# Kernel optimization log

Hardware: AMD Instinct MI355X
Metric: run time of the kernel (lower is better)

Reference implementation:

```python
import jax, jax.numpy as jnp
import numpy as np

N_NODES = 25000
N_HEDGES = 12500
NNZ = 400000
C_IN = 128
HID = 256
HEADS = 4
DH = HID // HEADS  # 64
NQ = 1             # number_queries
LN_EPS = 1e-5


def _layer_norm(x, g, b):
    m = jnp.mean(x, axis=-1, keepdims=True)
    v = jnp.mean((x - m) ** 2, axis=-1, keepdims=True)
    return (x - m) * jax.lax.rsqrt(v + LN_EPS) * g + b


def _block(x_src, src, tgt, n_tgt, K, Qw, V, ln0_g, ln0_b, ln1_g, ln1_b, W1, W2):
    """AllSetTransformerBlock: segment-softmax multi-head attention + LN/MLP.

    x_src: [N_src, C]; K,V: [H, C, DH]; Qw: [H, NQ, DH]; src,tgt: [E] int.
    torch.sparse.softmax over dim=1 == softmax over each target's incident
    sources (unspecified entries are -inf), so a segment softmax is exact.
    """
    xK = jnp.einsum('nc,hcd->hnd', x_src, K)        # [H, N, DH]
    alpha = jnp.einsum('hqd,hnd->nhq', Qw, xK)      # [N, H, NQ]
    a = alpha[src]                                   # [E, H, NQ] gather per incidence
    m = jax.ops.segment_max(a, tgt, num_segments=n_tgt)
    e = jnp.exp(a - m[tgt])
    den = jax.ops.segment_sum(e, tgt, num_segments=n_tgt)
    attn = e / den[tgt]                              # [E, H, NQ]
    v = jnp.einsum('nc,hcd->nhd', x_src, V)[src]     # [E, H, DH]
    w = attn[:, :, :, None] * v[:, :, None, :]       # [E, H, NQ, DH]
    out = jax.ops.segment_sum(w, tgt, num_segments=n_tgt)  # [T, H, NQ, DH]
    out = out + Qw[None]                             # residual with queries
    out = out.transpose(0, 2, 1, 3).reshape(n_tgt, NQ, HID)
    x = _layer_norm(out, ln0_g, ln0_b)
    h = jnp.maximum(x @ W1, 0.0) @ W2                # MLP: Linear-ReLU-Linear, no bias
    x = _layer_norm(x + jnp.maximum(h, 0.0), ln1_g, ln1_b)
    return x.sum(axis=1)                             # [T, HID]


def setup_inputs() -> dict:
    key = jax.random.key(0)
    ks = jax.random.split(key, 12)
    # injective linear-congruential index generation -> unique (node, hedge) pairs,
    # matching a coalesced sparse incidence matrix
    P = 15485863
    lin = (np.arange(NNZ, dtype=np.int64) * P) % (N_NODES * N_HEDGES)
    node_idx = jnp.asarray(lin // N_HEDGES, dtype=jnp.int64)
    hedge_idx = jnp.asarray(lin % N_HEDGES, dtype=jnp.int64)
    s = 0.05
    w = lambda k, shape: jax.random.normal(k, shape, jnp.float32) * s
    d = {
        'x0': jax.random.normal(ks[0], (N_NODES, C_IN), jnp.float32),
        'node_idx': node_idx,
        'hedge_idx': hedge_idx,
        'n_hedges': N_HEDGES,
        'v2e_K': w(ks[1], (HEADS, C_IN, DH)),
        'v2e_Q': w(ks[2], (HEADS, NQ, DH)),
        'v2e_V': w(ks[3], (HEADS, C_IN, DH)),
        'v2e_W1': w(ks[4], (HID, HID)),
        'v2e_W2': w(ks[5], (HID, HID)),
        'v2e_ln0_g': jnp.ones(HID, jnp.float32), 'v2e_ln0_b': jnp.zeros(HID, jnp.float32),
        'v2e_ln1_g': jnp.ones(HID, jnp.float32), 'v2e_ln1_b': jnp.zeros(HID, jnp.float32),
        'e2v_K': w(ks[6], (HEADS, HID, DH)),
        'e2v_Q': w(ks[7], (HEADS, NQ, DH)),
        'e2v_V': w(ks[8], (HEADS, HID, DH)),
        'e2v_W1': w(ks[9], (HID, HID)),
        'e2v_W2': w(ks[10], (HID, HID)),
        'e2v_ln0_g': jnp.ones(HID, jnp.float32), 'e2v_ln0_b': jnp.zeros(HID, jnp.float32),
        'e2v_ln1_g': jnp.ones(HID, jnp.float32), 'e2v_ln1_b': jnp.zeros(HID, jnp.float32),
    }
    return d


def reference(x0, node_idx, hedge_idx, n_hedges,
              v2e_K, v2e_Q, v2e_V, v2e_W1, v2e_W2,
              v2e_ln0_g, v2e_ln0_b, v2e_ln1_g, v2e_ln1_b,
              e2v_K, e2v_Q, e2v_V, e2v_W1, e2v_W2,
              e2v_ln0_g, e2v_ln0_b, e2v_ln1_g, e2v_ln1_b):
    n_nodes = x0.shape[0]
    # vertex -> hyperedge (neighborhood = B^T: targets are hyperedges)
    x1 = jax.nn.relu(_block(x0, node_idx, hedge_idx, n_hedges,
                            v2e_K, v2e_Q, v2e_V,
                            v2e_ln0_g, v2e_ln0_b, v2e_ln1_g, v2e_ln1_b,
                            v2e_W1, v2e_W2))
    # hyperedge -> vertex (neighborhood = B: targets are nodes)
    x0_out = jax.nn.relu(_block(x1, hedge_idx, node_idx, n_nodes,
                                e2v_K, e2v_Q, e2v_V,
                                e2v_ln0_g, e2v_ln0_b, e2v_ln1_g, e2v_ln1_b,
                                e2v_W1, e2v_W2))
    return x0_out, x1
```

## Files before the change

### kernel.cpp

```cpp
#include <hip/hip_runtime.h>
#include <hip/hip_bf16.h>

#define N_NODES_C 25000
#define N_HEDGES_C 12500
#define NNZ_C 400000
#define C_IN_C 128
#define HID_C 256
#define LN_EPS_C 1e-5f
#define CSR_STRIDE 64

typedef unsigned short ushort_t;
typedef __attribute__((ext_vector_type(8))) short short8;
typedef __attribute__((ext_vector_type(4))) float f32x4;

union U4S8 { uint4 u; short8 s; };

__device__ __forceinline__ float ldsel(const void* p, size_t i, bool f32) {
    return f32 ? ((const float*)p)[i] : __bfloat162float(((const __hip_bfloat16*)p)[i]);
}
__device__ __forceinline__ int ldidx(const void* p, size_t i, bool i64) {
    return i64 ? (int)((const long long*)p)[i] : ((const int*)p)[i];
}
__device__ __forceinline__ ushort_t bfbits(float f) {
    union { float f; unsigned u; } v; v.f = f;
    unsigned r = v.u + 0x7FFF + ((v.u >> 16) & 1);
    return (ushort_t)(r >> 16);
}
__device__ __forceinline__ float blo(unsigned u) {
    union { unsigned u; float f; } v; v.u = u << 16; return v.f;
}
__device__ __forceinline__ float bhi(unsigned u) {
    union { unsigned u; float f; } v; v.u = u & 0xFFFF0000u; return v.f;
}

#define INIT_GRID 3273
__global__ void __launch_bounds__(256)
init_kernel(const unsigned* __restrict__ x0w, const unsigned* __restrict__ idxw,
            int* __restrict__ flags, unsigned* __restrict__ cnts,
            unsigned* __restrict__ scsrh32, unsigned* __restrict__ scsrn32,
            unsigned* __restrict__ vb32, unsigned* __restrict__ ea32) {
    int bid = blockIdx.x;
    if (bid == 0) {
        __shared__ int cnt[2];
        int t = threadIdx.x;
        if (t < 2) cnt[t] = 0;
        __syncthreads();
        int c0 = 0, c1 = 0;
        for (int k = 0; k < 4; k++) {
            unsigned w = x0w[t * 4 + k];
            unsigned elo = (w >> 7) & 0xFF;
            if (elo >= 100 && elo <= 134) c0++;
            if (idxw[2 * (t * 4 + k) + 1] == 0) c1++;
        }
        atomicAdd(&cnt[0], c0);
        atomicAdd(&cnt[1], c1);
        __syncthreads();
        if (t == 0) {
            flags[0] = (cnt[0] < 512) ? 1 : 0;
            flags[1] = (cnt[1] >= 512) ? 1 : 0;
        }
        return;
    }
    int i = (bid - 1) * 256 + threadIdx.x;
    if (i < 37500) { cnts[i] = 0u; return; }
    i -= 37500;
    if (i < 400000) { scsrh32[i] = 0x61A861A8u; return; }
    i -= 400000;
    if (i < 400000) { scsrn32[i] = 0x30D430D4u; return; }
    i -= 400000;
    if (i < 128) { vb32[25000 * 128 + i] = 0u; return; }
    i -= 128;
    if (i < 4) ea32[100000 + i] = 0u;
}

#define PREP_TOTAL 364544
__global__ void prep_kernel(const void* __restrict__ K1, const void* __restrict__ Q1,
                            const void* __restrict__ V1,
                            const void* __restrict__ K2, const void* __restrict__ Q2,
                            const void* __restrict__ V2,
                            const void* __restrict__ W1a, const void* __restrict__ W2a,
                            const void* __restrict__ W1b, const void* __restrict__ W2b,
                            const void* __restrict__ G0a, const void* __restrict__ B0a,
                            const void* __restrict__ G1a, const void* __restrict__ B1a,
                            const void* __restrict__ G0b, const void* __restrict__ B0b,
                            const void* __restrict__ G1b, const void* __restrict__ B1b,
                            const int* __restrict__ flags,
                            float* __restrict__ kq1, float* __restrict__ kq2,
                            ushort_t* __restrict__ Vt1b, ushort_t* __restrict__ Vt2b,
                            ushort_t* __restrict__ W1tA, ushort_t* __restrict__ W2tA,
                            ushort_t* __restrict__ W1tB, ushort_t* __restrict__ W2tB,
                            float* __restrict__ qgb1, float* __restrict__ ep1,
                            float* __restrict__ qgb2, float* __restrict__ ep2) {
    bool f32 = flags[0] != 0;
    size_t i = (size_t)blockIdx.x * 256 + threadIdx.x;
    if (i >= PREP_TOTAL) return;
    if (i < 512) {
        int h = (int)(i >> 7), c = (int)(i & 127);
        float s = 0.f;
        for (int d = 0; d < 64; d++)
            s += ldsel(K1, (size_t)(h * 128 + c) * 64 + d, f32) * ldsel(Q1, h * 64 + d, f32);
        kq1[h * 128 + c] = s;
        return;
    }
    i -= 512;
    if (i < 1024) {
        int h = (int)(i >> 8), c = (int)(i & 255);
        float s = 0.f;
        for (int d = 0; d < 64; d++)
            s += ldsel(K2, (size_t)(h * 256 + c) * 64 + d, f32) * ldsel(Q2, h * 64 + d, f32);
        kq2[h * 256 + c] = s;
        return;
    }
    i -= 1024;
    if (i < 32768) {
        int j = (int)(i >> 7), c = (int)(i & 127);
        int h = j >> 6, d = j & 63;
        Vt1b[i] = bfbits(ldsel(V1, (size_t)(h * 128 + c) * 64 + d, f32));
        return;
    }
    i -= 32768;
    if (i < 65536) {
        int j = (int)(i >> 8), c = (int)(i & 255);
        int h = j >> 6, d = j & 63;
        Vt2b[i] = bfbits(ldsel(V2, (size_t)(h * 256 + c) * 64 + d, f32));
        return;
    }
    i -= 65536;
    if (i < 65536) { int n = (int)(i >> 8), k = (int)(i & 255);
        W1tA[i] = bfbits(ldsel(W1a, (size_t)k * 256 + n, f32)); return; }
    i -= 65536;
    if (i < 65536) { int n = (int)(i >> 8), k = (int)(i & 255);
        W2tA[i] = bfbits(ldsel(W2a, (size_t)k * 256 + n, f32)); return; }
    i -= 65536;
    if (i < 65536) { int n = (int)(i >> 8), k = (int)(i & 255);
        W1tB[i] = bfbits(ldsel(W1b, (size_t)k * 256 + n, f32)); return; }
    i -= 65536;
    if (i < 65536) { int n = (int)(i >> 8), k = (int)(i & 255);
        W2tB[i] = bfbits(ldsel(W2b, (size_t)k * 256 + n, f32)); return; }
    i -= 65536;
    {
        int which = (int)(i >> 8);
        int j = (int)(i & 255);
        const void* src; float* dst;
        switch (which) {
            case 0: src = Q1;  dst = qgb1;       break;
            case 1: src = G0a; dst = qgb1 + 256; break;
            case 2: src = B0a; dst = qgb1 + 512; break;
            case 3: src = G1a; dst = ep1;        break;
            case 4: src = B1a; dst = ep1 + 256;  break;
            case 5: src = Q2;  dst = qgb2;       break;
            case 6: src = G0b; dst = qgb2 + 256; break;
            case 7: src = B0b; dst = qgb2 + 512; break;
            case 8: src = G1b; dst = ep2;        break;
            default: src = B1b; dst = ep2 + 256;  break;
        }
        dst[j] = ldsel(src, j, f32);
    }
}

#define FILL_CHUNK 1024
#define FILL_NCHUNK ((NNZ_C + FILL_CHUNK - 1) / FILL_CHUNK)
#define HSLICE_SZ 1563
#define NSLICE_SZ 3125
__global__ void __launch_bounds__(256)
fill_kernel(const void* __restrict__ node_idx, const void* __restrict__ hedge_idx,
            const int* __restrict__ flags,
            int* __restrict__ fill_h, int* __restrict__ fill_n,
            ushort_t* __restrict__ scsr_h, ushort_t* __restrict__ scsr_n) {
    bool i64 = flags[1] != 0;
    int s = blockIdx.x & 7;
    int chunk = blockIdx.x >> 3;
    int e0 = chunk * FILL_CHUNK;
    int e1 = e0 + FILL_CHUNK; if (e1 > NNZ_C) e1 = NNZ_C;
    int hlo = s * HSLICE_SZ, hhi = hlo + HSLICE_SZ;
    int nlo = s * NSLICE_SZ, nhi = nlo + NSLICE_SZ;
    for (int e = e0 + threadIdx.x; e < e1; e += 256) {
        int nd = ldidx(node_idx, e, i64);
        int he = ldidx(hedge_idx, e, i64);
        if (he >= hlo && he < hhi) {
            int p = atomicAdd(&fill_h[he], 1);
            if (p < CSR_STRIDE) scsr_h[(he << 6) + p] = (ushort_t)nd;
        }
        if (nd >= nlo && nd < nhi) {
            int p = atomicAdd(&fill_n[nd], 1);
            if (p < CSR_STRIDE) scsr_n[(nd << 6) + p] = (ushort_t)he;
        }
    }
}

__device__ __forceinline__ void gemm_mfma_body(
    const ushort_t* __restrict__ Abf, const float* __restrict__ Af32,
    const ushort_t* __restrict__ Bt, ushort_t* __restrict__ Cout,
    int M, int K, int row0, int col0, int relu, ushort_t* As, ushort_t* Bs) {
    int tid = threadIdx.x;
    int w = tid >> 6, lane = tid & 63;
    int l15 = lane & 15, kg = lane >> 4;
    int wr = w >> 1, wc = w & 1;
    f32x4 acc[2][4] = {{{0.f,0.f,0.f,0.f},{0.f,0.f,0.f,0.f},{0.f,0.f,0.f,0.f},{0.f,0.f,0.f,0.f}},
                       {{0.f,0.f,0.f,0.f},{0.f,0.f,0.f,0.f},{0.f,0.f,0.f,0.f},{0.f,0.f,0.f,0.f}}};
    for (int k0 = 0; k0 < K; k0 += 64) {
#pragma unroll
        for (int p = 0; p < 2; p++) {
            int i = p * 256 + tid;
            int r = i >> 3, ch = i & 7;
            uint4 av = {0u,0u,0u,0u};
            int gr = row0 + r;
            if (gr < M) {
                if (Abf) {
                    av = *(const uint4*)(Abf + (size_t)gr * K + k0 + ch * 8);
                } else {
                    const float* ap = Af32 + (size_t)gr * K + k0 + ch * 8;
                    float4 f0 = *(const float4*)ap;
                    float4 f1 = *(const float4*)(ap + 4);
                    av.x = (unsigned)bfbits(f0.x) | ((unsigned)bfbits(f0.y) << 16);
                    av.y = (unsigned)bfbits(f0.z) | ((unsigned)bfbits(f0.w) << 16);
                    av.z = (unsigned)bfbits(f1.x) | ((unsigned)bfbits(f1.y) << 16);
                    av.w = (unsigned)bfbits(f1.z) | ((unsigned)bfbits(f1.w) << 16);
                }
            }
            *(uint4*)&As[r * 72 + ch * 8] = av;
        }
#pragma unroll
        for (int p = 0; p < 4; p++) {
            int i = p * 256 + tid;
            int r2 = i >> 3, c2 = i & 7;
            uint4 bv = *(const uint4*)(Bt + (size_t)(col0 + r2) * K + k0 + c2 * 8);
            *(uint4*)&Bs[r2 * 72 + c2 * 8] = bv;
        }
        __syncthreads();
#pragma unroll
        for (int kk = 0; kk < 2; kk++) {
            U4S8 a0_, a1_;
            a0_.u = *(const uint4*)&As[(32 * wr + l15) * 72 + kk * 32 + kg * 8];
            a1_.u = *(const uint4*)&As[(32 * wr + 16 + l15) * 72 + kk * 32 + kg * 8];
#pragma unroll
            for (int n = 0; n < 4; n++) {
                U4S8 b; b.u = *(const uint4*)&Bs[(64 * wc + 16 * n + l15) * 72 + kk * 32 + kg * 8];
                acc[0][n] = __builtin_amdgcn_mfma_f32_16x16x32_bf16(a0_.s, b.s, acc[0][n], 0, 0, 0);
                acc[1][n] = __builtin_amdgcn_mfma_f32_16x16x32_bf16(a1_.s, b.s, acc[1][n], 0, 0, 0);
            }
        }
        __syncthreads();
    }
#pragma unroll
    for (int m = 0; m < 2; m++) {
#pragma unroll
        for (int n = 0; n < 4; n++) {
#pragma unroll
            for (int rr = 0; rr < 4; rr++) {
                int row = row0 + 32 * wr + 16 * m + kg * 4 + rr;
                if (row < M) {
                    float v = acc[m][n][rr];
                    if (relu) v = fmaxf(v, 0.f);
                    Cout[(size_t)row * 256 + col0 + 64 * wc + 16 * n + l15] = bfbits(v);
                }
            }
        }
    }
}

__global__ void __launch_bounds__(256)
gemm_bf16_kernel(const ushort_t* __restrict__ A, const ushort_t* __restrict__ Bt,
                 ushort_t* __restrict__ C, int M, int K, int relu) {
    __shared__ ushort_t As[64 * 72];
    __shared__ ushort_t Bs[128 * 72];
    gemm_mfma_body(A, nullptr, Bt, C, M, K, blockIdx.x * 64, blockIdx.y * 128, relu, As, Bs);
}

__global__ void __launch_bounds__(256)
gemm_x0_kernel(const void* __restrict__ x0, const int* __restrict__ flags,
               const ushort_t* __restrict__ Bt, ushort_t* __restrict__ C,
               int M, int K) {
    __shared__ ushort_t As[64 * 72];
    __shared__ ushort_t Bs[128 * 72];
    bool f32 = flags[0] != 0;
    gemm_mfma_body(f32 ? nullptr : (const ushort_t*)x0,
                   f32 ? (const float*)x0 : nullptr,
                   Bt, C, M, K, blockIdx.x * 64, blockIdx.y * 128, 0, As, Bs);
}

__global__ void __launch_bounds__(512)
fused_mlp_ln_kernel(const ushort_t* __restrict__ A, const ushort_t* __restrict__ W1t,
                    const ushort_t* __restrict__ W2t, const float* __restrict__ ep,
                    float* __restrict__ outF, ushort_t* __restrict__ xbfOut, int M) {
    __shared__ ushort_t Bs[256 * 72];
    __shared__ ushort_t hs[64 * 264];
    __shared__ float s1s[64][4];
    __shared__ float s2s[64][4];
    ushort_t* As = hs;
    int tid = threadIdx.x;
    int w = tid >> 6, lane = tid & 63;
    int l15 = lane & 15, kg = lane >> 4;
    int wr = w >> 2, wc = w & 3;
    int row0 = blockIdx.x * 64;
    f32x4 acc[2][4] = {{{0.f,0.f,0.f,0.f},{0.f,0.f,0.f,0.f},{0.f,0.f,0.f,0.f},{0.f,0.f,0.f,0.f}},
                       {{0.f,0.f,0.f,0.f},{0.f,0.f,0.f,0.f},{0.f,0.f,0.f,0.f},{0.f,0.f,0.f,0.f}}};
    int r = tid >> 3, ch = tid & 7;
    for (int k0 = 0; k0 < 256; k0 += 64) {
        uint4 av = {0u,0u,0u,0u};
        int gr = row0 + r;
        if (gr < M) av = *(const uint4*)(A + (size_t)gr * 256 + k0 + ch * 8);
        *(uint4*)&As[r * 72 + ch * 8] = av;
#pragma unroll
        for (int p = 0; p < 4; p++) {
            int i = p * 512 + tid;
            int r2 = i >> 3, c2 = i & 7;
            uint4 bv = *(const uint4*)(W1t + (size_t)r2 * 256 + k0 + c2 * 8);
            *(uint4*)&Bs[r2 * 72 + c2 * 8] = bv;
        }
        __syncthreads();
#pragma unroll
        for (int kk = 0; kk < 2; kk++) {
            U4S8 a0_, a1_;
            a0_.u = *(const uint4*)&As[(32 * wr + l15) * 72 + kk * 32 + kg * 8];
            a1_.u = *(const uint4*)&As[(32 * wr + 16 + l15) * 72 + kk * 32 + kg * 8];
#pragma unroll
            for (int n = 0; n < 4; n++) {
                U4S8 b; b.u = *(const uint4*)&Bs[(64 * wc + 16 * n + l15) * 72 + kk * 32 + kg * 8];
                acc[0][n] = __builtin_amdgcn_mfma_f32_16x16x32_bf16(a0_.s, b.s, acc[0][n], 0, 0, 0);
                acc[1][n] = __builtin_amdgcn_mfma_f32_16x16x32_bf16(a1_.s, b.s, acc[1][n], 0, 0, 0);
            }
        }
        __syncthreads();
    }
#pragma unroll
    for (int m = 0; m < 2; m++) {
#pragma unroll
        for (int n = 0; n < 4; n++) {
#pragma unroll
            for (int rr = 0; rr < 4; rr++) {
                int br = 32 * wr + 16 * m + kg * 4 + rr;
                hs[br * 264 + 64 * wc + 16 * n + l15] = bfbits(fmaxf(acc[m][n][rr], 0.f));
                acc[m][n][rr] = 0.f;
            }
        }
    }
    __syncthreads();
    for (int k0 = 0; k0 < 256; k0 += 64) {
#pragma unroll
        for (int p = 0; p < 4; p++) {
            int i = p * 512 + tid;
            int r2 = i >> 3, c2 = i & 7;
            uint4 bv = *(const uint4*)(W2t + (size_t)r2 * 256 + k0 + c2 * 8);
            *(uint4*)&Bs[r2 * 72 + c2 * 8] = bv;
        }
        __syncthreads();
#pragma unroll
        for (int kk = 0; kk < 2; kk++) {
            U4S8 a0_, a1_;
            a0_.u = *(const uint4*)&hs[(32 * wr + l15) * 264 + k0 + kk * 32 + kg * 8];
            a1_.u = *(const uint4*)&hs[(32 * wr + 16 + l15) * 264 + k0 + kk * 32 + kg * 8];
#pragma unroll
            for (int n = 0; n < 4; n++) {
                U4S8 b; b.u = *(const uint4*)&Bs[(64 * wc + 16 * n + l15) * 72 + kk * 32 + kg * 8];
                acc[0][n] = __builtin_amdgcn_mfma_f32_16x16x32_bf16(a0_.s, b.s, acc[0][n], 0, 0, 0);
                acc[1][n] = __builtin_amdgcn_mfma_f32_16x16x32_bf16(a1_.s, b.s, acc[1][n], 0, 0, 0);
            }
        }
        __syncthreads();
    }
    float ym[2][4][4];
#pragma unroll
    for (int m = 0; m < 2; m++) {
#pragma unroll
        for (int rr = 0; rr < 4; rr++) {
            int br = 32 * wr + 16 * m + kg * 4 + rr;
            int grow = row0 + br;
            float ls1 = 0.f;
#pragma unroll
            for (int n = 0; n < 4; n++) {
                int col = 64 * wc + 16 * n + l15;
                float xv = 0.f;
                if (grow < M) xv = blo((unsigned)A[(size_t)grow * 256 + col]);
                float yv = xv + fmaxf(acc[m][n][rr], 0.f);
                ym[m][n][rr] = yv;
                ls1 += yv;
            }
#pragma unroll
            for (int msk = 1; msk < 16; msk <<= 1) ls1 += __shfl_xor(ls1, msk);
            if (l15 == 0) s1s[br][wc] = ls1;
        }
    }
    __syncthreads();
    float mean_[2][4];
#pragma unroll
    for (int m = 0; m < 2; m++) {
#pragma unroll
        for (int rr = 0; rr < 4; rr++) {
            int br = 32 * wr + 16 * m + kg * 4 + rr;
            float mn = (s1s[br][0] + s1s[br][1] + s1s[br][2] + s1s[br][3]) * (1.f / 256.f);
            mean_[m][rr] = mn;
            float ls2 = 0.f;
#pragma unroll
            for (int n = 0; n < 4; n++) {
                float d = ym[m][n][rr] - mn;
                ls2 += d * d;
            }
#pragma unroll
            for (int msk = 1; msk < 16; msk <<= 1) ls2 += __shfl_xor(ls2, msk);
            if (l15 == 0) s2s[br][wc] = ls2;
        }
    }
    __syncthreads();
#pragma unroll
    for (int m = 0; m < 2; m++) {
#pragma unroll
        for (int rr = 0; rr < 4; rr++) {
            int br = 32 * wr + 16 * m + kg * 4 + rr;
            int grow = row0 + br;
            float var = (s2s[br][0] + s2s[br][1] + s2s[br][2] + s2s[br][3]) * (1.f / 256.f);
            float rs = rsqrtf(var + LN_EPS_C);
            if (grow < M) {
#pragma unroll
                for (int n = 0; n < 4; n++) {
                    int col = 64 * wc + 16 * n + l15;
                    float rv = (ym[m][n][rr] - mean_[m][rr]) * rs * ep[col] + ep[256 + col];
                    rv = fmaxf(rv, 0.f);
                    outF[(size_t)grow * 256 + col] = rv;
                    if (xbfOut) xbfOut[(size_t)grow * 256 + col] = bfbits(rv);
                }
            }
        }
    }
}

__global__ void __launch_bounds__(256)
expalpha_kernel(const void* __restrict__ x, int mode,
                const int* __restrict__ flags,
                const float* __restrict__ kq,
                float* __restrict__ ea, int M, int C,
                unsigned* __restrict__ zrow, float* __restrict__ zea) {
    __shared__ float kqs[1024];
    if (blockIdx.x == gridDim.x - 1) {
        int t = threadIdx.x;
        if (zrow) {
            if (t < 128) zrow[t] = 0u;
            else if (t < 132) zea[t - 128] = 0.f;
        }
        return;
    }
    bool xf32 = mode ? false : (flags[0] != 0);
    for (int i = threadIdx.x; i < 4 * C; i += 256) kqs[i] = kq[i];
    __syncthreads();
    int lane = threadIdx.x & 63;
    int n = blockIdx.x * 4 + (threadIdx.x >> 6);
    if (n >= M) return;
    float s0, s1, s2, s3;
    if (xf32) {
        float2 v = *(const float2*)((const float*)x + (size_t)n * C + lane * 2);
        int c = lane * 2;
        s0 = v.x * kqs[c]         + v.y * kqs[c + 1];
        s1 = v.x * kqs[C + c]     + v.y * kqs[C + c + 1];
        s2 = v.x * kqs[2 * C + c] + v.y * kqs[2 * C + c + 1];
        s3 = v.x * kqs[3 * C + c] + v.y * kqs[3 * C + c + 1];
    } else if (C == 128) {
        unsigned u = *((const unsigned*)x + (size_t)n * 64 + lane);
        float xl = blo(u), xh = bhi(u);
        int c = lane * 2;
        s0 = xl * kqs[c]         + xh * kqs[c + 1];
        s1 = xl * kqs[C + c]     + xh * kqs[C + c + 1];
        s2 = xl * kqs[2 * C + c] + xh * kqs[2 * C + c + 1];
        s3 = xl * kqs[3 * C + c] + xh * kqs[3 * C + c + 1];
    } else {
        uint2 u = *((const uint2*)x + (size_t)n * 64 + lane);
        float x0v = blo(u.x), x1v = bhi(u.x), x2v = blo(u.y), x3v = bhi(u.y);
        int c = lane * 4;
        s0 = x0v * kqs[c]         + x1v * kqs[c + 1]         + x2v * kqs[c + 2]         + x3v * kqs[c + 3];
        s1 = x0v * kqs[C + c]     + x1v * kqs[C + c + 1]     + x2v * kqs[C + c + 2]     + x3v * kqs[C + c + 3];
        s2 = x0v * kqs[2 * C + c] + x1v * kqs[2 * C + c + 1] + x2v * kqs[2 * C + c + 2] + x3v * kqs[2 * C + c + 3];
        s3 = x0v * kqs[3 * C + c] + x1v * kqs[3 * C + c + 1] + x2v * kqs[3 * C + c + 2] + x3v * kqs[3 * C + c + 3];
    }
#pragma unroll
    for (int m = 32; m; m >>= 1) {
        s0 += __shfl_xor(s0, m);
        s1 += __shfl_xor(s1, m);
        s2 += __shfl_xor(s2, m);
        s3 += __shfl_xor(s3, m);
    }
    if (lane == 0) {
        float4 o;
        o.x = __expf(s0); o.y = __expf(s1); o.z = __expf(s2); o.w = __expf(s3);
        *(float4*)(ea + (size_t)n * 4) = o;
    }
}

#define DECL_BANKD(B) float e##B##0, e##B##1, e##B##2, e##B##3; \
                      uint2 u##B##0, u##B##1, u##B##2, u##B##3;
#define ISSUED1(B, n, sl) { int _o = __shfl(myidx, (sl)) << 9; \
    u##B##n = *(const uint2*)(vbL + _o); \
    e##B##n = *(const float*)(eaL + (_o >> 5)); }
#define ISSUED4(B, base) ISSUED1(B,0,(base)) ISSUED1(B,1,(base)+1) ISSUED1(B,2,(base)+2) ISSUED1(B,3,(base)+3)
#define EATD1(B, n) { \
    float wgt = e##B##n; \
    den += wgt; \
    a0 += wgt * blo(u##B##n.x); a1 += wgt * bhi(u##B##n.x); \
    a2 += wgt * blo(u##B##n.y); a3 += wgt * bhi(u##B##n.y); }
#define EATD4(B) EATD1(B,0) EATD1(B,1) EATD1(B,2) EATD1(B,3)

__global__ void __launch_bounds__(256)
attn_ln_kernel(const int* __restrict__ cnts, const ushort_t* __restrict__ scsr,
               const char* __restrict__ eaB, const char* __restrict__ vbB,
               const float* __restrict__ qgb, uint2* __restrict__ xlnbf2) {
    int wid = (blockIdx.x << 2) + (threadIdx.x >> 6);
    int lane = threadIdx.x & 63;
    const char* vbL = vbB + (lane << 3);
    const char* eaL = eaB + ((lane >> 4) << 2);
    int cnt = cnts[wid];
    if (cnt > CSR_STRIDE) cnt = CSR_STRIDE;
    int myidx = (int)scsr[(wid << 6) + lane];
    float a0 = 0.f, a1 = 0.f, a2 = 0.f, a3 = 0.f, den = 0.f;
    int kr = (cnt + 3) & ~3;
    DECL_BANKD(A)
    DECL_BANKD(B)
    if (kr > 0) { ISSUED4(A, 0) }
    for (int k = 0; k < kr; k += 8) {
        int kb = k + 4;
        bool hasB = kb < kr;
        if (hasB) { ISSUED4(B, kb) }
        EATD4(A)
        int ka = k + 8;
        if (ka < kr) { ISSUED4(A, ka) }
        if (hasB) { EATD4(B) }
    }
    float inv = (den > 0.f) ? (1.f / den) : 0.f;
    int c0i = lane << 2;
    float o0 = a0 * inv + qgb[c0i];
    float o1 = a1 * inv + qgb[c0i + 1];
    float o2 = a2 * inv + qgb[c0i + 2];
    float o3 = a3 * inv + qgb[c0i + 3];
    float part = o0 + o1 + o2 + o3;
#pragma unroll
    for (int m = 32; m; m >>= 1) part += __shfl_xor(part, m);
    float mean = part * (1.f / 256.f);
    float d0 = o0 - mean, d1 = o1 - mean, d2 = o2 - mean, d3 = o3 - mean;
    float p2 = d0 * d0 + d1 * d1 + d2 * d2 + d3 * d3;
#pragma unroll
    for (int m = 32; m; m >>= 1) p2 += __shfl_xor(p2, m);
    float rs = rsqrtf(p2 * (1.f / 256.f) + LN_EPS_C);
    float r0 = d0 * rs * qgb[256 + c0i] + qgb[512 + c0i];
    float r1 = d1 * rs * qgb[256 + c0i + 1] + qgb[512 + c0i + 1];
    float r2 = d2 * rs * qgb[256 + c0i + 2] + qgb[512 + c0i + 2];
    float r3 = d3 * rs * qgb[256 + c0i + 3] + qgb[512 + c0i + 3];
    uint2 outw;
    outw.x = ((unsigned)bfbits(r1) << 16) | bfbits(r0);
    outw.y = ((unsigned)bfbits(r3) << 16) | bfbits(r2);
    xlnbf2[(size_t)wid * 64 + lane] = outw;
}

#define OFF_KQ1   0
#define OFF_KQ2   2048
#define OFF_QGB1  6144
#define OFF_EP1   9216
#define OFF_QGB2  11264
#define OFF_EP2   14336
#define OFF_EA    16384
#define OFF_VT1B  416512
#define OFF_VT2B  482048
#define OFF_W1TA  613120
#define OFF_W2TA  744192
#define OFF_W1TB  875264
#define OFF_W2TB  1006336
#define OFF_VB    1137408
#define OFF_XLNBF 13937920
#define OFF_H1    26737920
#define OFF_X1BF  39537920
#define OFF_FLAGS 45937920
#define OFF_FILLH 45937952
#define OFF_FILLN 45987952
#define OFF_SCSRH 46087952
#define OFF_SCSRN 47687952

extern "C" void kernel_launch(void* const* d_in, const int* in_sizes, int n_in,
                              void* d_out, int out_size, void* d_ws, size_t ws_size,
                              hipStream_t stream) {
    const void* x0        = d_in[0];
    const void* node_idx  = d_in[1];
    const void* hedge_idx = d_in[2];
    const void* v2e_K  = d_in[4];
    const void* v2e_Q  = d_in[5];
    const void* v2e_V  = d_in[6];
    const void* v2e_W1 = d_in[7];
    const void* v2e_W2 = d_in[8];
    const void* v2e_ln0_g = d_in[9];
    const void* v2e_ln0_b = d_in[10];
    const void* v2e_ln1_g = d_in[11];
    const void* v2e_ln1_b = d_in[12];
    const void* e2v_K  = d_in[13];
    const void* e2v_Q  = d_in[14];
    const void* e2v_V  = d_in[15];
    const void* e2v_W1 = d_in[16];
    const void* e2v_W2 = d_in[17];
    const void* e2v_ln0_g = d_in[18];
    const void* e2v_ln0_b = d_in[19];
    const void* e2v_ln1_g = d_in[20];
    const void* e2v_ln1_b = d_in[21];

    float* out = (float*)d_out;
    float* out_x0 = out;
    float* out_x1 = out + (size_t)N_NODES_C * HID_C;

    char* base = (char*)d_ws;
    float*    kq1   = (float*)(base + OFF_KQ1);
    float*    kq2   = (float*)(base + OFF_KQ2);
    float*    qgb1  = (float*)(base + OFF_QGB1);
    float*    ep1   = (float*)(base + OFF_EP1);
    float*    qgb2  = (float*)(base + OFF_QGB2);
    float*    ep2   = (float*)(base + OFF_EP2);
    float*    ea    = (float*)(base + OFF_EA);
    ushort_t* Vt1b  = (ushort_t*)(base + OFF_VT1B);
    ushort_t* Vt2b  = (ushort_t*)(base + OFF_VT2B);
    ushort_t* W1tA  = (ushort_t*)(base + OFF_W1TA);
    ushort_t* W2tA  = (ushort_t*)(base + OFF_W2TA);
    ushort_t* W1tB  = (ushort_t*)(base + OFF_W1TB);
    ushort_t* W2tB  = (ushort_t*)(base + OFF_W2TB);
    ushort_t* vb    = (ushort_t*)(base + OFF_VB);
    ushort_t* xlnbf = (ushort_t*)(base + OFF_XLNBF);
    ushort_t* x1bf  = (ushort_t*)(base + OFF_X1BF);
    int*      flags = (int*)(base + OFF_FLAGS);
    int*      fill_h = (int*)(base + OFF_FILLH);
    int*      fill_n = (int*)(base + OFF_FILLN);
    ushort_t* scsr_h = (ushort_t*)(base + OFF_SCSRH);
    ushort_t* scsr_n = (ushort_t*)(base + OFF_SCSRN);

    init_kernel<<<INIT_GRID, 256, 0, stream>>>(
        (const unsigned*)x0, (const unsigned*)node_idx, flags,
        (unsigned*)fill_h, (unsigned*)scsr_h, (unsigned*)scsr_n,
        (unsigned*)vb, (unsigned*)ea);

    prep_kernel<<<(PREP_TOTAL + 255) / 256, 256, 0, stream>>>(
        v2e_K, v2e_Q, v2e_V, e2v_K, e2v_Q, e2v_V,
        v2e_W1, v2e_W2, e2v_W1, e2v_W2,
        v2e_ln0_g, v2e_ln0_b, v2e_ln1_g, v2e_ln1_b,
        e2v_ln0_g, e2v_ln0_b, e2v_ln1_g, e2v_ln1_b,
        flags, kq1, kq2, Vt1b, Vt2b, W1tA, W2tA, W1tB, W2tB,
        qgb1, ep1, qgb2, ep2);

    fill_kernel<<<8 * FILL_NCHUNK, 256, 0, stream>>>(
        node_idx, hedge_idx, flags, fill_h, fill_n, scsr_h, scsr_n);

    gemm_x0_kernel<<<dim3((N_NODES_C + 63) / 64, 2), 256, 0, stream>>>(
        x0, flags, Vt1b, vb, N_NODES_C, C_IN_C);
    expalpha_kernel<<<N_NODES_C / 4 + 1, 256, 0, stream>>>(
        x0, 0, flags, kq1, ea, N_NODES_C, C_IN_C, nullptr, nullptr);
    attn_ln_kernel<<<N_HEDGES_C / 4, 256, 0, stream>>>(
        fill_h, scsr_h, (const char*)ea, (const char*)vb, qgb1, (uint2*)xlnbf);
    fused_mlp_ln_kernel<<<(N_HEDGES_C + 63) / 64, 512, 0, stream>>>(
        xlnbf, W1tA, W2tA, ep1, out_x1, x1bf, N_HEDGES_C);

    gemm_bf16_kernel<<<dim3((N_HEDGES_C + 63) / 64, 2), 256, 0, stream>>>(
        x1bf, Vt2b, vb, N_HEDGES_C, 256, 0);
    expalpha_kernel<<<N_HEDGES_C / 4 + 1, 256, 0, stream>>>(
        x1bf, 1, flags, kq2, ea, N_HEDGES_C, HID_C,
        (unsigned*)vb + 12500 * 128, ea + 50000);
    attn_ln_kernel<<<N_NODES_C / 4, 256, 0, stream>>>(
        fill_n, scsr_n, (const char*)ea, (const char*)vb, qgb2, (uint2*)xlnbf);
    fused_mlp_ln_kernel<<<(N_NODES_C + 63) / 64, 512, 0, stream>>>(
        xlnbf, W1tB, W2tB, ep2, out_x0, nullptr, N_NODES_C);
}
```

Measured before the change: 218.0 us.

## Fuse exp-alpha into GEMMs and chain second-block V projection into MLP kernel

Computes the per-row attention logits and exp for the first block inside the x0 GEMM's A-tile loads, so the separate expalpha kernel is no longer needed. In the first block's fused MLP/LN kernel, the LN output is kept in shared memory as bf16. That same kernel then computes the second block's exp-alpha and the V projection GEMM directly. This removes three kernel launches and the x1bf round trip through global memory. In exchange the fused kernel carries more shared memory and serial work per block, and the y==0 GEMM blocks do extra scalar dot products.

```diff
diff --git a/kernel.cpp b/kernel.cpp
--- a/kernel.cpp
+++ b/kernel.cpp
@@ -188,34 +188,64 @@
     }
 }
 
-__device__ __forceinline__ void gemm_mfma_body(
-    const ushort_t* __restrict__ Abf, const float* __restrict__ Af32,
-    const ushort_t* __restrict__ Bt, ushort_t* __restrict__ Cout,
-    int M, int K, int row0, int col0, int relu, ushort_t* As, ushort_t* Bs) {
+__global__ void __launch_bounds__(256)
+gemm_x0_kernel(const void* __restrict__ x0, const int* __restrict__ flags,
+               const ushort_t* __restrict__ Bt, ushort_t* __restrict__ C,
+               int M, int K, const float* __restrict__ kq, float* __restrict__ ea) {
+    __shared__ ushort_t As[64 * 72];
+    __shared__ ushort_t Bs[128 * 72];
+    __shared__ float kqs[512];
+    bool f32 = flags[0] != 0;
     int tid = threadIdx.x;
     int w = tid >> 6, lane = tid & 63;
     int l15 = lane & 15, kg = lane >> 4;
     int wr = w >> 1, wc = w & 1;
+    int row0 = blockIdx.x * 64, col0 = blockIdx.y * 128;
+    bool doEa = (blockIdx.y == 0);
+    kqs[tid] = kq[tid];
+    kqs[256 + tid] = kq[256 + tid];
+    __syncthreads();
     f32x4 acc[2][4] = {{{0.f,0.f,0.f,0.f},{0.f,0.f,0.f,0.f},{0.f,0.f,0.f,0.f},{0.f,0.f,0.f,0.f}},
                        {{0.f,0.f,0.f,0.f},{0.f,0.f,0.f,0.f},{0.f,0.f,0.f,0.f},{0.f,0.f,0.f,0.f}}};
+    float hd[2][4] = {{0.f,0.f,0.f,0.f},{0.f,0.f,0.f,0.f}};
+    int r_ = tid >> 3, ch = tid & 7;
     for (int k0 = 0; k0 < K; k0 += 64) {
 #pragma unroll
         for (int p = 0; p < 2; p++) {
-            int i = p * 256 + tid;
-            int r = i >> 3, ch = i & 7;
+            int r = p * 32 + r_;
             uint4 av = {0u,0u,0u,0u};
             int gr = row0 + r;
             if (gr < M) {
-                if (Abf) {
-                    av = *(const uint4*)(Abf + (size_t)gr * K + k0 + ch * 8);
+                float fv[8];
+                if (!f32) {
+                    av = *(const uint4*)((const ushort_t*)x0 + (size_t)gr * K + k0 + ch * 8);
+                    if (doEa) {
+                        unsigned* uw = (unsigned*)&av;
+#pragma unroll
+                        for (int jj = 0; jj < 4; jj++) { fv[2 * jj] = blo(uw[jj]); fv[2 * jj + 1] = bhi(uw[jj]); }
+                    }
                 } else {
-                    const float* ap = Af32 + (size_t)gr * K + k0 + ch * 8;
+                    const float* ap = (const float*)x0 + (size_t)gr * K + k0 + ch * 8;
                     float4 f0 = *(const float4*)ap;
                     float4 f1 = *(const float4*)(ap + 4);
                     av.x = (unsigned)bfbits(f0.x) | ((unsigned)bfbits(f0.y) << 16);
                     av.y = (unsigned)bfbits(f0.z) | ((unsigned)bfbits(f0.w) << 16);
                     av.z = (unsigned)bfbits(f1.x) | ((unsigned)bfbits(f1.y) << 16);
                     av.w = (unsigned)bfbits(f1.z) | ((unsigned)bfbits(f1.w) << 16);
+                    if (doEa) {
+                        fv[0] = f0.x; fv[1] = f0.y; fv[2] = f0.z; fv[3] = f0.w;
+                        fv[4] = f1.x; fv[5] = f1.y; fv[6] = f1.z; fv[7] = f1.w;
+                    }
+                }
+                if (doEa) {
+                    int c = k0 + ch * 8;
+#pragma unroll
+                    for (int h = 0; h < 4; h++) {
+                        float s = 0.f;
+#pragma unroll
+                        for (int j = 0; j < 8; j++) s += fv[j] * kqs[h * 128 + c + j];
+                        hd[p][h] += s;
+                    }
                 }
             }
             *(uint4*)&As[r * 72 + ch * 8] = av;
@@ -249,50 +279,54 @@
 #pragma unroll
             for (int rr = 0; rr < 4; rr++) {
                 int row = row0 + 32 * wr + 16 * m + kg * 4 + rr;
+                if (row < M)
+                    C[(size_t)row * 256 + col0 + 64 * wc + 16 * n + l15] = bfbits(acc[m][n][rr]);
+            }
+        }
+    }
+    if (doEa) {
+#pragma unroll
+        for (int p = 0; p < 2; p++) {
+#pragma unroll
+            for (int msk = 1; msk < 8; msk <<= 1) {
+                hd[p][0] += __shfl_xor(hd[p][0], msk);
+                hd[p][1] += __shfl_xor(hd[p][1], msk);
+                hd[p][2] += __shfl_xor(hd[p][2], msk);
+                hd[p][3] += __shfl_xor(hd[p][3], msk);
+            }
+            if (ch == 0) {
+                int row = row0 + p * 32 + r_;
                 if (row < M) {
-                    float v = acc[m][n][rr];
-                    if (relu) v = fmaxf(v, 0.f);
-                    Cout[(size_t)row * 256 + col0 + 64 * wc + 16 * n + l15] = bfbits(v);
+                    float4 o;
+                    o.x = __expf(hd[p][0]); o.y = __expf(hd[p][1]);
+                    o.z = __expf(hd[p][2]); o.w = __expf(hd[p][3]);
+                    *(float4*)(ea + (size_t)row * 4) = o;
                 }
             }
         }
     }
-}
-
-__global__ void __launch_bounds__(256)
-gemm_bf16_kernel(const ushort_t* __restrict__ A, const ushort_t* __restrict__ Bt,
-                 ushort_t* __restrict__ C, int M, int K, int relu) {
-    __shared__ ushort_t As[64 * 72];
-    __shared__ ushort_t Bs[128 * 72];
-    gemm_mfma_body(A, nullptr, Bt, C, M, K, blockIdx.x * 64, blockIdx.y * 128, relu, As, Bs);
-}
-
-__global__ void __launch_bounds__(256)
-gemm_x0_kernel(const void* __restrict__ x0, const int* __restrict__ flags,
-               const ushort_t* __restrict__ Bt, ushort_t* __restrict__ C,
-               int M, int K) {
-    __shared__ ushort_t As[64 * 72];
-    __shared__ ushort_t Bs[128 * 72];
-    bool f32 = flags[0] != 0;
-    gemm_mfma_body(f32 ? nullptr : (const ushort_t*)x0,
-                   f32 ? (const float*)x0 : nullptr,
-                   Bt, C, M, K, blockIdx.x * 64, blockIdx.y * 128, 0, As, Bs);
 }
 
 __global__ void __launch_bounds__(512)
 fused_mlp_ln_kernel(const ushort_t* __restrict__ A, const ushort_t* __restrict__ W1t,
                     const ushort_t* __restrict__ W2t, const float* __restrict__ ep,
-                    float* __restrict__ outF, ushort_t* __restrict__ xbfOut, int M) {
+                    float* __restrict__ outF, int M,
+                    const ushort_t* __restrict__ Vt2b, const float* __restrict__ kq,
+                    ushort_t* __restrict__ vbOut, float* __restrict__ eaOut,
+                    unsigned* __restrict__ zrow, float* __restrict__ zea) {
     __shared__ ushort_t Bs[256 * 72];
     __shared__ ushort_t hs[64 * 264];
     __shared__ float s1s[64][4];
     __shared__ float s2s[64][4];
+    __shared__ float kqs[1024];
     ushort_t* As = hs;
     int tid = threadIdx.x;
     int w = tid >> 6, lane = tid & 63;
     int l15 = lane & 15, kg = lane >> 4;
     int wr = w >> 2, wc = w & 3;
     int row0 = blockIdx.x * 64;
+    bool dir1 = (Vt2b != nullptr);
+    if (dir1) { kqs[tid] = kq[tid]; kqs[512 + tid] = kq[512 + tid]; }
     f32x4 acc[2][4] = {{{0.f,0.f,0.f,0.f},{0.f,0.f,0.f,0.f},{0.f,0.f,0.f,0.f},{0.f,0.f,0.f,0.f}},
                        {{0.f,0.f,0.f,0.f},{0.f,0.f,0.f,0.f},{0.f,0.f,0.f,0.f},{0.f,0.f,0.f,0.f}}};
     int r = tid >> 3, ch = tid & 7;
@@ -410,77 +444,91 @@
             int grow = row0 + br;
             float var = (s2s[br][0] + s2s[br][1] + s2s[br][2] + s2s[br][3]) * (1.f / 256.f);
             float rs = rsqrtf(var + LN_EPS_C);
-            if (grow < M) {
-#pragma unroll
-                for (int n = 0; n < 4; n++) {
-                    int col = 64 * wc + 16 * n + l15;
-                    float rv = (ym[m][n][rr] - mean_[m][rr]) * rs * ep[col] + ep[256 + col];
-                    rv = fmaxf(rv, 0.f);
-                    outF[(size_t)grow * 256 + col] = rv;
-                    if (xbfOut) xbfOut[(size_t)grow * 256 + col] = bfbits(rv);
-                }
-            }
-        }
-    }
-}
-
-__global__ void __launch_bounds__(256)
-expalpha_kernel(const void* __restrict__ x, int mode,
-                const int* __restrict__ flags,
-                const float* __restrict__ kq,
-                float* __restrict__ ea, int M, int C,
-                unsigned* __restrict__ zrow, float* __restrict__ zea) {
-    __shared__ float kqs[1024];
-    if (blockIdx.x == gridDim.x - 1) {
-        int t = threadIdx.x;
-        if (zrow) {
-            if (t < 128) zrow[t] = 0u;
-            else if (t < 132) zea[t - 128] = 0.f;
-        }
-        return;
-    }
-    bool xf32 = mode ? false : (flags[0] != 0);
-    for (int i = threadIdx.x; i < 4 * C; i += 256) kqs[i] = kq[i];
+#pragma unroll
+            for (int n = 0; n < 4; n++) {
+                int col = 64 * wc + 16 * n + l15;
+                float rv = (ym[m][n][rr] - mean_[m][rr]) * rs * ep[col] + ep[256 + col];
+                rv = fmaxf(rv, 0.f);
+                if (grow < M) outF[(size_t)grow * 256 + col] = rv;
+                if (dir1) hs[br * 264 + col] = bfbits(rv);
+            }
+        }
+    }
+    if (!dir1) return;
+#pragma unroll
+    for (int m = 0; m < 2; m++)
+#pragma unroll
+        for (int n = 0; n < 4; n++)
+#pragma unroll
+            for (int rr = 0; rr < 4; rr++) acc[m][n][rr] = 0.f;
     __syncthreads();
-    int lane = threadIdx.x & 63;
-    int n = blockIdx.x * 4 + (threadIdx.x >> 6);
-    if (n >= M) return;
-    float s0, s1, s2, s3;
-    if (xf32) {
-        float2 v = *(const float2*)((const float*)x + (size_t)n * C + lane * 2);
-        int c = lane * 2;
-        s0 = v.x * kqs[c]         + v.y * kqs[c + 1];
-        s1 = v.x * kqs[C + c]     + v.y * kqs[C + c + 1];
-        s2 = v.x * kqs[2 * C + c] + v.y * kqs[2 * C + c + 1];
-        s3 = v.x * kqs[3 * C + c] + v.y * kqs[3 * C + c + 1];
-    } else if (C == 128) {
-        unsigned u = *((const unsigned*)x + (size_t)n * 64 + lane);
-        float xl = blo(u), xh = bhi(u);
-        int c = lane * 2;
-        s0 = xl * kqs[c]         + xh * kqs[c + 1];
-        s1 = xl * kqs[C + c]     + xh * kqs[C + c + 1];
-        s2 = xl * kqs[2 * C + c] + xh * kqs[2 * C + c + 1];
-        s3 = xl * kqs[3 * C + c] + xh * kqs[3 * C + c + 1];
-    } else {
-        uint2 u = *((const uint2*)x + (size_t)n * 64 + lane);
-        float x0v = blo(u.x), x1v = bhi(u.x), x2v = blo(u.y), x3v = bhi(u.y);
-        int c = lane * 4;
-        s0 = x0v * kqs[c]         + x1v * kqs[c + 1]         + x2v * kqs[c + 2]         + x3v * kqs[c + 3];
-        s1 = x0v * kqs[C + c]     + x1v * kqs[C + c + 1]     + x2v * kqs[C + c + 2]     + x3v * kqs[C + c + 3];
-        s2 = x0v * kqs[2 * C + c] + x1v * kqs[2 * C + c + 1] + x2v * kqs[2 * C + c + 2] + x3v * kqs[2 * C + c + 3];
-        s3 = x0v * kqs[3 * C + c] + x1v * kqs[3 * C + c + 1] + x2v * kqs[3 * C + c + 2] + x3v * kqs[3 * C + c + 3];
-    }
-#pragma unroll
-    for (int m = 32; m; m >>= 1) {
-        s0 += __shfl_xor(s0, m);
-        s1 += __shfl_xor(s1, m);
-        s2 += __shfl_xor(s2, m);
-        s3 += __shfl_xor(s3, m);
-    }
-    if (lane == 0) {
-        float4 o;
-        o.x = __expf(s0); o.y = __expf(s1); o.z = __expf(s2); o.w = __expf(s3);
-        *(float4*)(ea + (size_t)n * 4) = o;
+    if (blockIdx.x == 0) {
+        if (tid < 128) zrow[tid] = 0u;
+        else if (tid < 132) zea[tid - 128] = 0.f;
+    }
+    {
+        int rrow = tid >> 3, rch = tid & 7;
+        float h0 = 0.f, h1 = 0.f, h2 = 0.f, h3 = 0.f;
+#pragma unroll
+        for (int q = 0; q < 4; q++) {
+            uint4 xv = *(const uint4*)&hs[rrow * 264 + rch * 32 + q * 8];
+            const unsigned* uw = (const unsigned*)&xv;
+#pragma unroll
+            for (int jj = 0; jj < 4; jj++) {
+                float xl = blo(uw[jj]), xh = bhi(uw[jj]);
+                int c = rch * 32 + q * 8 + jj * 2;
+                h0 += xl * kqs[c]       + xh * kqs[c + 1];
+                h1 += xl * kqs[256 + c] + xh * kqs[256 + c + 1];
+                h2 += xl * kqs[512 + c] + xh * kqs[512 + c + 1];
+                h3 += xl * kqs[768 + c] + xh * kqs[768 + c + 1];
+            }
+        }
+#pragma unroll
+        for (int msk = 1; msk < 8; msk <<= 1) {
+            h0 += __shfl_xor(h0, msk); h1 += __shfl_xor(h1, msk);
+            h2 += __shfl_xor(h2, msk); h3 += __shfl_xor(h3, msk);
+        }
+        int grow = row0 + rrow;
+        if (rch == 0 && grow < M) {
+            float4 o;
+            o.x = __expf(h0); o.y = __expf(h1); o.z = __expf(h2); o.w = __expf(h3);
+            *(float4*)(eaOut + (size_t)grow * 4) = o;
+        }
+    }
+    for (int k0 = 0; k0 < 256; k0 += 64) {
+#pragma unroll
+        for (int p = 0; p < 4; p++) {
+            int i = p * 512 + tid;
+            int r2 = i >> 3, c2 = i & 7;
+            uint4 bv = *(const uint4*)(Vt2b + (size_t)r2 * 256 + k0 + c2 * 8);
+            *(uint4*)&Bs[r2 * 72 + c2 * 8] = bv;
+        }
+        __syncthreads();
+#pragma unroll
+        for (int kk = 0; kk < 2; kk++) {
+            U4S8 a0_, a1_;
+            a0_.u = *(const uint4*)&hs[(32 * wr + l15) * 264 + k0 + kk * 32 + kg * 8];
+            a1_.u = *(const uint4*)&hs[(32 * wr + 16 + l15) * 264 + k0 + kk * 32 + kg * 8];
+#pragma unroll
+            for (int n = 0; n < 4; n++) {
+                U4S8 b; b.u = *(const uint4*)&Bs[(64 * wc + 16 * n + l15) * 72 + kk * 32 + kg * 8];
+                acc[0][n] = __builtin_amdgcn_mfma_f32_16x16x32_bf16(a0_.s, b.s, acc[0][n], 0, 0, 0);
+                acc[1][n] = __builtin_amdgcn_mfma_f32_16x16x32_bf16(a1_.s, b.s, acc[1][n], 0, 0, 0);
+            }
+        }
+        __syncthreads();
+    }
+#pragma unroll
+    for (int m = 0; m < 2; m++) {
+#pragma unroll
+        for (int n = 0; n < 4; n++) {
+#pragma unroll
+            for (int rr = 0; rr < 4; rr++) {
+                int row = row0 + 32 * wr + 16 * m + kg * 4 + rr;
+                if (row < M)
+                    vbOut[(size_t)row * 256 + 64 * wc + 16 * n + l15] = bfbits(acc[m][n][rr]);
+            }
+        }
     }
 }
 
@@ -562,8 +610,6 @@
 #define OFF_W2TB  1006336
 #define OFF_VB    1137408
 #define OFF_XLNBF 13937920
-#define OFF_H1    26737920
-#define OFF_X1BF  39537920
 #define OFF_FLAGS 45937920
 #define OFF_FILLH 45937952
 #define OFF_FILLN 45987952
@@ -615,7 +661,6 @@
     ushort_t* W2tB  = (ushort_t*)(base + OFF_W2TB);
     ushort_t* vb    = (ushort_t*)(base + OFF_VB);
     ushort_t* xlnbf = (ushort_t*)(base + OFF_XLNBF);
-    ushort_t* x1bf  = (ushort_t*)(base + OFF_X1BF);
     int*      flags = (int*)(base + OFF_FLAGS);
     int*      fill_h = (int*)(base + OFF_FILLH);
     int*      fill_n = (int*)(base + OFF_FILLN);
@@ -639,21 +684,17 @@
         node_idx, hedge_idx, flags, fill_h, fill_n, scsr_h, scsr_n);
 
     gemm_x0_kernel<<<dim3((N_NODES_C + 63) / 64, 2), 256, 0, stream>>>(
-        x0, flags, Vt1b, vb, N_NODES_C, C_IN_C);
-    expalpha_kernel<<<N_NODES_C / 4 + 1, 256, 0, stream>>>(
-        x0, 0, flags, kq1, ea, N_NODES_C, C_IN_C, nullptr, nullptr);
+        x0, flags, Vt1b, vb, N_NODES_C, C_IN_C, kq1, ea);
     attn_ln_kernel<<<N_HEDGES_C / 4, 256, 0, stream>>>(
         fill_h, scsr_h, (const char*)ea, (const char*)vb, qgb1, (uint2*)xlnbf);
     fused_mlp_ln_kernel<<<(N_HEDGES_C + 63) / 64, 512, 0, stream>>>(
-        xlnbf, W1tA, W2tA, ep1, out_x1, x1bf, N_HEDGES_C);
-
-    gemm_bf16_kernel<<<dim3((N_HEDGES_C + 63) / 64, 2), 256, 0, stream>>>(
-        x1bf, Vt2b, vb, N_HEDGES_C, 256, 0);
-    expalpha_kernel<<<N_HEDGES_C / 4 + 1, 256, 0, stream>>>(
-        x1bf, 1, flags, kq2, ea, N_HEDGES_C, HID_C,
+        xlnbf, W1tA, W2tA, ep1, out_x1, N_HEDGES_C,
+        Vt2b, kq2, vb, ea,
         (unsigned*)vb + 12500 * 128, ea + 50000);
+
     attn_ln_kernel<<<N_NODES_C / 4, 256, 0, stream>>>(
         fill_n, scsr_n, (const char*)ea, (const char*)vb, qgb2, (uint2*)xlnbf);
     fused_mlp_ln_kernel<<<(N_NODES_C + 63) / 64, 512, 0, stream>>>(
-        xlnbf, W1tB, W2tB, ep2, out_x0, nullptr, N_NODES_C);
-}
+        xlnbf, W1tB, W2tB, ep2, out_x0, N_NODES_C,
+        nullptr, nullptr, nullptr, nullptr, nullptr, nullptr);
+}
```

Result: faster. 190.9 us (-12.4%).
